# Kernel optimization log

Measured on AMD Instinct MI355X. Metric: run time of the kernel, lower is better.

The kernel has to match this reference:

```python
import jax, jax.numpy as jnp
import numpy as np

EPS = 1e-06

def _splat_dists(t, centers):
    # t: [B,T,H,Dh], centers: [H,S,Dh] -> euclidean dists [B,T,H,S] (torch.cdist)
    t_sq = jnp.sum(t * t, axis=-1, keepdims=True)          # [B,T,H,1]
    c_sq = jnp.sum(centers * centers, axis=-1)             # [H,S]
    dots = jnp.einsum('bthd,hsd->bths', t, centers)        # [B,T,H,S]
    d2 = jnp.maximum(t_sq + c_sq[None, None] - 2.0 * dots, 0.0)
    return jnp.sqrt(d2)


def setup_inputs() -> dict:
    key = jax.random.key(0)
    ks = jax.random.split(key, 6)
    B, T, D, H, S = 2, 2048, 1024, 8, 32
    Dh = D // H
    scale = 1.0 / np.sqrt(D)
    return {
        'x': jax.random.normal(ks[0], (B, T, D), jnp.float32),
        'Wqkv': jax.random.normal(ks[1], (D, 3 * D), jnp.float32) * scale,
        'bqkv': jnp.zeros((3 * D,), jnp.float32),
        'Wout': jax.random.normal(ks[2], (D, D), jnp.float32) * scale,
        'bout': jnp.zeros((D,), jnp.float32),
        'splat_centers': jax.random.normal(ks[3], (H, S, Dh), jnp.float32) * 0.5,
        'splat_log_scales': jnp.zeros((H, S), jnp.float32),
        'splat_log_amplitudes': jnp.zeros((H, S), jnp.float32),
        'temperature': jnp.ones((1,), jnp.float32),
    }


def reference(x, Wqkv, bqkv, Wout, bout, splat_centers, splat_log_scales,
              splat_log_amplitudes, temperature):
    B, T, D = x.shape
    H, S, Dh = splat_centers.shape
    qkv = (x @ Wqkv + bqkv).reshape(B, T, 3, H, Dh)
    q, k, v = qkv[:, :, 0], qkv[:, :, 1], qkv[:, :, 2]     # [B,T,H,Dh]

    q_dists = _splat_dists(q, splat_centers)               # [B,T,H,S]
    k_dists = _splat_dists(k, splat_centers)               # [B,T,H,S]

    scales = jnp.exp(splat_log_scales)[None, None]         # [1,1,H,S]
    q_weights = jnp.exp(-0.5 * (q_dists / (scales + EPS)) ** 2)
    k_weights = jnp.exp(-0.5 * (k_dists / (scales + EPS)) ** 2)

    amplitudes = jnp.exp(splat_log_amplitudes)             # [H,S]
    # bihs,bjhs,hs -> bijh : fold amplitudes into q_weights first
    qa = q_weights * amplitudes[None, None]
    logits = jnp.einsum('bihs,bjhs->bijh', qa, k_weights) / temperature[0]
    attention = jax.nn.softmax(logits, axis=2)             # softmax over j
    out = jnp.einsum('bijh,bjhd->bihd', attention, v).reshape(B, T, D)
    return out @ Wout + bout, attention
```

## Files before the change

kernel.cpp:

```cpp
#include <hip/hip_runtime.h>
#include <math.h>


typedef __attribute__((ext_vector_type(8))) short s16x8;
typedef __attribute__((ext_vector_type(4))) short s16x4;
typedef __attribute__((ext_vector_type(4))) float f32x4;

__device__ inline short f2bf(float f) {
  union { float f; unsigned u; } v; v.f = f;
  unsigned r = v.u + 0x7FFFu + ((v.u >> 16) & 1u);
  return (short)(r >> 16);
}
__device__ inline float bf2f(short s) {
  union { unsigned u; float f; } v;
  v.u = ((unsigned)(unsigned short)s) << 16;
  return v.f;
}
__device__ inline unsigned cvt_pk_bf16(float lo, float hi) {
  unsigned r;
  asm("v_cvt_pk_bf16_f32 %0, %1, %2" : "=v"(r) : "v"(lo), "v"(hi));
  return r;
}
#define MFMA_BF16(a, b, c) __builtin_amdgcn_mfma_f32_16x16x32_bf16((a), (b), (c), 0, 0, 0)

#define GLOAD_LDS16(gsrc, ldst)                                          \
  __builtin_amdgcn_global_load_lds(                                      \
      (const __attribute__((address_space(1))) void*)(gsrc),             \
      (__attribute__((address_space(3))) void*)(ldst), 16, 0, 0)

__device__ inline void transpose_tile32(const float* __restrict__ W,
                                        short* __restrict__ Wt, int K, int N,
                                        int n0, int k0) {
  __shared__ float tile[32][33];
  const int r = threadIdx.x >> 3, c4 = (threadIdx.x & 7) * 4;
  float4 v = *(const float4*)(W + (size_t)(k0 + r) * N + n0 + c4);
  tile[r][c4 + 0] = v.x; tile[r][c4 + 1] = v.y;
  tile[r][c4 + 2] = v.z; tile[r][c4 + 3] = v.w;
  __syncthreads();
  s16x4 o;
  o[0] = f2bf(tile[c4 + 0][r]);
  o[1] = f2bf(tile[c4 + 1][r]);
  o[2] = f2bf(tile[c4 + 2][r]);
  o[3] = f2bf(tile[c4 + 3][r]);
  *(s16x4*)(Wt + (size_t)(n0 + r) * K + k0 + c4) = o;
}

__global__ __launch_bounds__(256) void prep_fused(
    const float* __restrict__ x, short* __restrict__ x16,
    const float* __restrict__ Wqkv, short* __restrict__ Wqt16,
    const float* __restrict__ Wout, short* __restrict__ Wot16,
    const float* __restrict__ ctr, const float* __restrict__ ls,
    const float* __restrict__ la, short* __restrict__ c16,
    float* __restrict__ csq, float* __restrict__ inv2, float* __restrict__ amp) {
  const int bx = blockIdx.x;
  if (bx < 4096) {
    int i = bx * 256 + threadIdx.x;
    float4 v = ((const float4*)x)[i];
    s16x4 o;
    o[0] = f2bf(v.x); o[1] = f2bf(v.y); o[2] = f2bf(v.z); o[3] = f2bf(v.w);
    ((s16x4*)x16)[i] = o;
  } else if (bx < 7168) {
    int idx = bx - 4096;
    transpose_tile32(Wqkv, Wqt16, 1024, 3072, (idx % 96) * 32, (idx / 96) * 32);
  } else if (bx < 8192) {
    int idx = bx - 7168;
    transpose_tile32(Wout, Wot16, 1024, 1024, (idx % 32) * 32, (idx / 32) * 32);
  } else {
    const int t = threadIdx.x;
    float sumsq = 0.f;
#pragma unroll
    for (int d = 0; d < 128; d += 4) {
      float4 v = *(const float4*)(ctr + (size_t)t * 128 + d);
      sumsq += v.x * v.x + v.y * v.y + v.z * v.z + v.w * v.w;
      s16x4 o;
      o[0] = f2bf(v.x); o[1] = f2bf(v.y); o[2] = f2bf(v.z); o[3] = f2bf(v.w);
      *(s16x4*)(c16 + (size_t)t * 128 + d) = o;
    }
    csq[t] = sumsq;
    float sc = __expf(ls[t]);
    float iv = 1.0f / (sc + 1e-6f);
    inv2[t] = -0.5f * iv * iv;
    amp[t] = __expf(la[t]);
  }
}

template <int N, bool SCATTER>
__global__ __launch_bounds__(256) void gemm_bf16(
    const short* __restrict__ A, const short* __restrict__ Wt,
    const float* __restrict__ bias,
    short* __restrict__ q16, short* __restrict__ k16, short* __restrict__ vt16,
    float* __restrict__ outf) {
  __shared__ union {
    struct { short As[128 * 64]; short Bs[128 * 64]; } s;
    short tv[128 * 136];
  } sm;
  const int tid = threadIdx.x;
  const int w = tid >> 6, l = tid & 63;
  const int lm = l & 15, lk = l >> 4;
  const int bn0 = blockIdx.x * 128;
  const int bm0 = blockIdx.y * 128;
  const int n0 = bn0 + (w & 1) * 64;
  const int m0 = bm0 + (w >> 1) * 64;
  const int K = 1024;
  f32x4 acc[4][4];
#pragma unroll
  for (int mi = 0; mi < 4; mi++)
#pragma unroll
    for (int ni = 0; ni < 4; ni++) acc[mi][ni] = (f32x4){0.f, 0.f, 0.f, 0.f};

  const int srow = l >> 3;
  const int scol = (l & 7) * 8;
  const int mh = (w >> 1) * 64, nh = (w & 1) * 64;

  for (int k0 = 0; k0 < K; k0 += 64) {
#pragma unroll
    for (int q = 0; q < 4; q++) {
      const int chunk = w * 4 + q;
      const int row = chunk * 8 + srow;
      GLOAD_LDS16(A + (size_t)(bm0 + row) * K + k0 + scol, sm.s.As + chunk * 512);
      GLOAD_LDS16(Wt + (size_t)(bn0 + row) * K + k0 + scol, sm.s.Bs + chunk * 512);
    }
    __syncthreads();
#pragma unroll
    for (int kk = 0; kk < 2; kk++) {
      s16x8 af[4], bf[4];
#pragma unroll
      for (int i = 0; i < 4; i++) {
        af[i] = *(const s16x8*)(sm.s.As + (mh + i * 16 + lm) * 64 + kk * 32 + lk * 8);
        bf[i] = *(const s16x8*)(sm.s.Bs + (nh + i * 16 + lm) * 64 + kk * 32 + lk * 8);
      }
#pragma unroll
      for (int mi = 0; mi < 4; mi++)
#pragma unroll
        for (int ni = 0; ni < 4; ni++)
          acc[mi][ni] = MFMA_BF16(af[mi], bf[ni], acc[mi][ni]);
    }
    __syncthreads();
  }
  if (SCATTER) {
    const int three = bn0 >> 10;
    if (three < 2) {
      short* dst0 = three ? k16 : q16;
      const int h = (bn0 >> 7) & 7;
      const int bb = bm0 >> 11;
      const int bh = bb * 8 + h;
      const int tt0 = bm0 & 2047;
#pragma unroll
      for (int ni = 0; ni < 4; ni++) {
        const int n = n0 + ni * 16 + lm;
        const int dh = n & 127;
        const float bv = bias[n];
#pragma unroll
        for (int mi = 0; mi < 4; mi++) {
#pragma unroll
          for (int r = 0; r < 4; r++) {
            const int ml = mh + mi * 16 + lk * 4 + r;
            dst0[((size_t)bh * 2048 + tt0 + ml) * 128 + dh] =
                f2bf(acc[mi][ni][r] + bv);
          }
        }
      }
    } else {
      const int h = (bn0 >> 7) & 7;
      const int bb = bm0 >> 11;
      const int bh = bb * 8 + h;
      const int tt0 = bm0 & 2047;
#pragma unroll
      for (int ni = 0; ni < 4; ni++) {
        const int nl = nh + ni * 16 + lm;
        const float bv = bias[bn0 + nl];
#pragma unroll
        for (int mi = 0; mi < 4; mi++) {
          const int ml = mh + mi * 16 + lk * 4;
          s16x4 o;
          o[0] = f2bf(acc[mi][ni][0] + bv);
          o[1] = f2bf(acc[mi][ni][1] + bv);
          o[2] = f2bf(acc[mi][ni][2] + bv);
          o[3] = f2bf(acc[mi][ni][3] + bv);
          *(s16x4*)(sm.tv + nl * 136 + ml) = o;
        }
      }
      __syncthreads();
#pragma unroll
      for (int c = 0; c < 8; c++) {
        const int u = c * 256 + tid;
        const int n = u >> 4, ch = u & 15;
        s16x8 vv = *(const s16x8*)(sm.tv + n * 136 + ch * 8);
        *(s16x8*)(vt16 + ((size_t)(bh * 128 + n)) * 2048 + tt0 + ch * 8) = vv;
      }
    }
  } else {
#pragma unroll
    for (int ni = 0; ni < 4; ni++) {
      const int n = n0 + ni * 16 + lm;
      const float bv = bias[n];
#pragma unroll
      for (int mi = 0; mi < 4; mi++) {
#pragma unroll
        for (int r = 0; r < 4; r++) {
          const int m = m0 + mi * 16 + lk * 4 + r;
          outf[(size_t)m * N + n] = acc[mi][ni][r] + bv;
        }
      }
    }
  }
}

__global__ __launch_bounds__(256) void splat_tv(
    const short* __restrict__ q16, const short* __restrict__ k16,
    const short* __restrict__ c16, const float* __restrict__ csq,
    const float* __restrict__ inv2, const float* __restrict__ amp,
    short* __restrict__ qa16, short* __restrict__ kw16) {
  const int tid = threadIdx.x;
  const int it = blockIdx.x & 31;
  const int bh = (blockIdx.x >> 5) & 15;
  const int which = blockIdx.x >> 9;
  const int w = tid >> 6, l = tid & 63;
  const int lm = l & 15, lk = l >> 4;
  const int h = bh & 7;
  const int i0 = it * 64 + w * 16;
  const short* src = which ? k16 : q16;

  s16x8 af[4];
  float sq = 0.f;
#pragma unroll
  for (int kk = 0; kk < 4; kk++) {
    af[kk] = *(const s16x8*)(src + ((size_t)bh * 2048 + i0 + lm) * 128 + kk * 32 + lk * 8);
#pragma unroll
    for (int j = 0; j < 8; j++) {
      float f = bf2f(af[kk][j]);
      sq += f * f;
    }
  }
  sq += __shfl_xor(sq, 16);
  sq += __shfl_xor(sq, 32);

  f32x4 acc[2];
  acc[0] = (f32x4){0.f, 0.f, 0.f, 0.f};
  acc[1] = (f32x4){0.f, 0.f, 0.f, 0.f};
#pragma unroll
  for (int kk = 0; kk < 4; kk++) {
    s16x8 b0 = *(const s16x8*)(c16 + (size_t)(h * 32 + lm) * 128 + kk * 32 + lk * 8);
    s16x8 b1 = *(const s16x8*)(c16 + (size_t)(h * 32 + 16 + lm) * 128 + kk * 32 + lk * 8);
    acc[0] = MFMA_BF16(af[kk], b0, acc[0]);
    acc[1] = MFMA_BF16(af[kk], b1, acc[1]);
  }
  short* dst = which ? kw16 : qa16;
#pragma unroll
  for (int ni = 0; ni < 2; ni++) {
    const int n = ni * 16 + lm;
    const float cs = csq[h * 32 + n];
    const float iv2 = inv2[h * 32 + n];
    const float am = which ? 1.0f : amp[h * 32 + n];
#pragma unroll
    for (int r = 0; r < 4; r++) {
      float qs = __shfl(sq, lk * 4 + r);
      float d2 = fmaxf(qs + cs - 2.0f * acc[ni][r], 0.0f);
      float wv = __expf(iv2 * d2) * am;
      int m = i0 + lk * 4 + r;
      dst[((size_t)bh * 2048 + m) * 32 + n] = f2bf(wv);
    }
  }
}

__global__ __launch_bounds__(256) void attn_flash(
    const short* __restrict__ qa16, const short* __restrict__ kw16,
    const short* __restrict__ vt16, const float* __restrict__ temp,
    float* __restrict__ lrow, short* __restrict__ aout16) {
  __shared__ short Vs[2][8192];
  const int tid = threadIdx.x;
  const int w = tid >> 6, l = tid & 63;
  const int lm = l & 15, lk = l >> 4;
  const int it = blockIdx.x, h = blockIdx.y;
  const int b = blockIdx.z;
  const int bh = b * 8 + h;
  const int i0 = it * 64 + w * 16;
  const float invT = 1.0f / temp[0];
  const short* kwb = kw16 + (size_t)bh * 2048 * 32;
  const short* vtb = vt16 + (size_t)bh * 128 * 2048;
  s16x8 qfrag = *(const s16x8*)(qa16 + ((size_t)(bh * 2048 + i0 + lm)) * 32 + lk * 8);
  float lsum = 0.f;
  f32x4 acc[8];
#pragma unroll
  for (int d = 0; d < 8; d++) acc[d] = (f32x4){0.f, 0.f, 0.f, 0.f};

  const int sig0 = (lm >> 2) * 8 + (lm & 3);
  const int srow8 = l >> 3;
  const int scb = (l & 7) ^ srow8;
  const int rcb0 = (lk ^ (lm & 7)) * 8;
  const int rcb1 = ((lk + 4) ^ (lm & 7)) * 8;

#pragma unroll
  for (int q = 0; q < 4; q++) {
    const int chunk = w * 4 + q;
    GLOAD_LDS16(vtb + (size_t)(chunk * 8 + srow8) * 2048 + scb * 8,
                &Vs[0][chunk * 512]);
  }
  __syncthreads();

  int cur = 0;
  for (int jc = 0; jc < 2048; jc += 64) {
    if (jc + 64 < 2048) {
#pragma unroll
      for (int q = 0; q < 4; q++) {
        const int chunk = w * 4 + q;
        GLOAD_LDS16(vtb + (size_t)(chunk * 8 + srow8) * 2048 + (jc + 64) + scb * 8,
                    &Vs[cur ^ 1][chunk * 512]);
      }
    }
    s16x8 kb[4];
    kb[0] = *(const s16x8*)(kwb + (size_t)(jc + sig0) * 32 + lk * 8);
    kb[1] = *(const s16x8*)(kwb + (size_t)(jc + sig0 + 4) * 32 + lk * 8);
    kb[2] = *(const s16x8*)(kwb + (size_t)(jc + sig0 + 32) * 32 + lk * 8);
    kb[3] = *(const s16x8*)(kwb + (size_t)(jc + sig0 + 36) * 32 + lk * 8);
    f32x4 z = (f32x4){0.f, 0.f, 0.f, 0.f};
    f32x4 s[4];
#pragma unroll
    for (int c = 0; c < 4; c++) s[c] = MFMA_BF16(kb[c], qfrag, z);
    float p[4][4];
#pragma unroll
    for (int c = 0; c < 4; c++) {
      p[c][0] = __expf(s[c][0] * invT);
      p[c][1] = __expf(s[c][1] * invT);
      p[c][2] = __expf(s[c][2] * invT);
      p[c][3] = __expf(s[c][3] * invT);
      lsum += (p[c][0] + p[c][1]) + (p[c][2] + p[c][3]);
    }
    union { unsigned u[4]; s16x8 v; } t0, t1;
    t0.u[0] = cvt_pk_bf16(p[0][0], p[0][1]);
    t0.u[1] = cvt_pk_bf16(p[0][2], p[0][3]);
    t0.u[2] = cvt_pk_bf16(p[1][0], p[1][1]);
    t0.u[3] = cvt_pk_bf16(p[1][2], p[1][3]);
    t1.u[0] = cvt_pk_bf16(p[2][0], p[2][1]);
    t1.u[1] = cvt_pk_bf16(p[2][2], p[2][3]);
    t1.u[2] = cvt_pk_bf16(p[3][0], p[3][1]);
    t1.u[3] = cvt_pk_bf16(p[3][2], p[3][3]);
    s16x8 pf0 = t0.v, pf1 = t1.v;
    const short* vb = Vs[cur];
#pragma unroll
    for (int d = 0; d < 8; d++) {
      const short* vsrow = vb + (d * 16 + lm) * 64;
      s16x8 vb0 = *(const s16x8*)(vsrow + rcb0);
      s16x8 vb1 = *(const s16x8*)(vsrow + rcb1);
      acc[d] = MFMA_BF16(pf0, vb0, acc[d]);
      acc[d] = MFMA_BF16(pf1, vb1, acc[d]);
    }
    __syncthreads();
    cur ^= 1;
  }
  lsum += __shfl_xor(lsum, 16);
  lsum += __shfl_xor(lsum, 32);
  if (l < 16) lrow[bh * 2048 + i0 + l] = lsum;
  float invl[4];
#pragma unroll
  for (int r = 0; r < 4; r++) invl[r] = 1.0f / __shfl(lsum, lk * 4 + r);
  short* ob = aout16 + ((size_t)(b * 2048 + i0)) * 1024 + h * 128 + lm;
#pragma unroll
  for (int r = 0; r < 4; r++) {
    const int row = lk * 4 + r;
#pragma unroll
    for (int d = 0; d < 8; d++)
      ob[(size_t)row * 1024 + d * 16] = f2bf(acc[d][r] * invl[r]);
  }
}

__global__ __launch_bounds__(256) void gemm_out(
    const short* __restrict__ aout16, const short* __restrict__ Wot16,
    const float* __restrict__ bout, float* __restrict__ out) {
  __shared__ short As[128 * 64];
  __shared__ short Bs[64 * 64];
  const int tid = threadIdx.x;
  const int w = tid >> 6, l = tid & 63;
  const int lm = l & 15, lk = l >> 4;
  const int idx = blockIdx.x;
  const int bn0 = (idx & 15) * 64;
  const int bm0 = (idx >> 4) * 128;
  const int K = 1024;
  f32x4 acc[4][2];
#pragma unroll
  for (int mi = 0; mi < 4; mi++)
#pragma unroll
    for (int ni = 0; ni < 2; ni++) acc[mi][ni] = (f32x4){0.f, 0.f, 0.f, 0.f};
  const int srow = l >> 3;
  const int scol = (l & 7) * 8;
  const int mh = (w >> 1) * 64, nh = (w & 1) * 32;
  for (int k0 = 0; k0 < K; k0 += 64) {
#pragma unroll
    for (int q = 0; q < 4; q++) {
      const int chunk = w * 4 + q;
      GLOAD_LDS16(aout16 + (size_t)(bm0 + chunk * 8 + srow) * K + k0 + scol,
                  As + chunk * 512);
    }
#pragma unroll
    for (int q = 0; q < 2; q++) {
      const int chunk = w * 2 + q;
      GLOAD_LDS16(Wot16 + (size_t)(bn0 + chunk * 8 + srow) * K + k0 + scol,
                  Bs + chunk * 512);
    }
    __syncthreads();
#pragma unroll
    for (int kk = 0; kk < 2; kk++) {
      s16x8 af[4], bf[2];
#pragma unroll
      for (int i = 0; i < 4; i++)
        af[i] = *(const s16x8*)(As + (mh + i * 16 + lm) * 64 + kk * 32 + lk * 8);
#pragma unroll
      for (int i = 0; i < 2; i++)
        bf[i] = *(const s16x8*)(Bs + (nh + i * 16 + lm) * 64 + kk * 32 + lk * 8);
#pragma unroll
      for (int mi = 0; mi < 4; mi++)
#pragma unroll
        for (int ni = 0; ni < 2; ni++)
          acc[mi][ni] = MFMA_BF16(af[mi], bf[ni], acc[mi][ni]);
    }
    __syncthreads();
  }
#pragma unroll
  for (int ni = 0; ni < 2; ni++) {
    const int n = bn0 + nh + ni * 16 + lm;
    const float bv = bout[n];
#pragma unroll
    for (int mi = 0; mi < 4; mi++) {
#pragma unroll
      for (int r = 0; r < 4; r++) {
        const int m = bm0 + mh + mi * 16 + lk * 4 + r;
        out[(size_t)m * 1024 + n] = acc[mi][ni][r] + bv;
      }
    }
  }
}

__global__ __launch_bounds__(256) void attn_write(
    const short* __restrict__ qa16, const short* __restrict__ kw16,
    const float* __restrict__ lrow, const float* __restrict__ temp,
    float* __restrict__ attn) {
  __shared__ float pl[8][16][33];
  const int tid = threadIdx.x;
  const int w = tid >> 6, l = tid & 63;
  const int lm = l & 15, lk = l >> 4;
  const int bx = blockIdx.x;
  const int i0 = (bx & 127) * 16;
  const int j0 = ((bx >> 7) & 63) * 32;
  const int b = bx >> 13;
  const float invT = 1.0f / temp[0];
#pragma unroll
  for (int hh = 0; hh < 2; hh++) {
    const int h = w * 2 + hh;
    const int bh = b * 8 + h;
    s16x8 qf = *(const s16x8*)(qa16 + ((size_t)(bh * 2048 + i0 + lm)) * 32 + lk * 8);
    s16x8 kf[2];
#pragma unroll
    for (int jh = 0; jh < 2; jh++)
      kf[jh] = *(const s16x8*)(kw16 + ((size_t)(bh * 2048 + j0 + jh * 16 + lm)) * 32 + lk * 8);
    float il[4];
#pragma unroll
    for (int r = 0; r < 4; r++)
      il[r] = 1.0f / lrow[bh * 2048 + i0 + lk * 4 + r];
    f32x4 z = (f32x4){0.f, 0.f, 0.f, 0.f};
#pragma unroll
    for (int jh = 0; jh < 2; jh++) {
      f32x4 s = MFMA_BF16(qf, kf[jh], z);
#pragma unroll
      for (int r = 0; r < 4; r++) {
        float p = __expf(s[r] * invT) * il[r];
        pl[h][lk * 4 + r][jh * 16 + lm] = p;
      }
    }
  }
  __syncthreads();
#pragma unroll
  for (int c = 0; c < 4; c++) {
    int u = c * 256 + tid;
    int i = u >> 6, rem = u & 63;
    int j = rem >> 1, h4 = (rem & 1) * 4;
    f32x4 v;
    v[0] = pl[h4][i][j];
    v[1] = pl[h4 + 1][i][j];
    v[2] = pl[h4 + 2][i][j];
    v[3] = pl[h4 + 3][i][j];
    f32x4* dst = (f32x4*)(attn + (((size_t)(b * 2048 + i0 + i)) * 2048 + j0 + j) * 8 + h4);
    __builtin_nontemporal_store(v, dst);
  }
}

extern "C" void kernel_launch(void* const* d_in, const int* in_sizes, int n_in,
                              void* d_out, int out_size, void* d_ws, size_t ws_size,
                              hipStream_t stream) {
  const float* x    = (const float*)d_in[0];
  const float* Wqkv = (const float*)d_in[1];
  const float* bqkv = (const float*)d_in[2];
  const float* Wout = (const float*)d_in[3];
  const float* bout = (const float*)d_in[4];
  const float* ctr  = (const float*)d_in[5];
  const float* ls   = (const float*)d_in[6];
  const float* la   = (const float*)d_in[7];
  const float* temp = (const float*)d_in[8];

  float* out = (float*)d_out;
  float* attn = out + 4194304;

  short* ws16 = (short*)d_ws;
  short* q16   = ws16;
  short* k16   = q16 + 4194304;
  short* vt16  = k16 + 4194304;
  short* x16   = vt16 + 4194304;
  short* Wqt16 = x16 + 4194304;
  short* Wot16 = Wqt16 + 3145728;
  short* qa16  = Wot16 + 1048576;
  short* kw16  = qa16 + 1048576;
  short* aout16 = kw16 + 1048576;
  short* c16   = aout16 + 4194304;
  float* lrow  = (float*)(c16 + 32768);
  float* csq   = lrow + 32768;
  float* inv2  = csq + 256;
  float* amp   = inv2 + 256;

  prep_fused<<<8193, 256, 0, stream>>>(x, x16, Wqkv, Wqt16, Wout, Wot16,
                                       ctr, ls, la, c16, csq, inv2, amp);
  gemm_bf16<3072, true><<<dim3(24, 32), 256, 0, stream>>>(
      x16, Wqt16, bqkv, q16, k16, vt16, nullptr);
  splat_tv<<<1024, 256, 0, stream>>>(
      q16, k16, c16, csq, inv2, amp, qa16, kw16);
  attn_flash<<<dim3(32, 8, 2), 256, 0, stream>>>(
      qa16, kw16, vt16, temp, lrow, aout16);
  gemm_out<<<512, 256, 0, stream>>>(aout16, Wot16, bout, out);
  attn_write<<<16384, 256, 0, stream>>>(qa16, kw16, lrow, temp, attn);
}
```

Before: 453.8 us.

## Fuse splat distance/weight computation into QKV GEMM epilogue

```diff
diff --git a/kernel.cpp b/kernel.cpp
--- a/kernel.cpp
+++ b/kernel.cpp
@@ -84,12 +84,13 @@
   }
 }
 
-template <int N, bool SCATTER>
-__global__ __launch_bounds__(256) void gemm_bf16(
+__global__ __launch_bounds__(256) void gemm_qkv(
     const short* __restrict__ A, const short* __restrict__ Wt,
     const float* __restrict__ bias,
-    short* __restrict__ q16, short* __restrict__ k16, short* __restrict__ vt16,
-    float* __restrict__ outf) {
+    const short* __restrict__ c16, const float* __restrict__ csq,
+    const float* __restrict__ inv2, const float* __restrict__ amp,
+    short* __restrict__ qa16, short* __restrict__ kw16,
+    short* __restrict__ vt16) {
   __shared__ union {
     struct { short As[128 * 64]; short Bs[128 * 64]; } s;
     short tv[128 * 136];
@@ -99,8 +100,6 @@
   const int lm = l & 15, lk = l >> 4;
   const int bn0 = blockIdx.x * 128;
   const int bm0 = blockIdx.y * 128;
-  const int n0 = bn0 + (w & 1) * 64;
-  const int m0 = bm0 + (w >> 1) * 64;
   const int K = 1024;
   f32x4 acc[4][4];
 #pragma unroll
@@ -137,128 +136,94 @@
     }
     __syncthreads();
   }
-  if (SCATTER) {
-    const int three = bn0 >> 10;
-    if (three < 2) {
-      short* dst0 = three ? k16 : q16;
-      const int h = (bn0 >> 7) & 7;
-      const int bb = bm0 >> 11;
-      const int bh = bb * 8 + h;
-      const int tt0 = bm0 & 2047;
-#pragma unroll
-      for (int ni = 0; ni < 4; ni++) {
-        const int n = n0 + ni * 16 + lm;
-        const int dh = n & 127;
-        const float bv = bias[n];
-#pragma unroll
-        for (int mi = 0; mi < 4; mi++) {
-#pragma unroll
-          for (int r = 0; r < 4; r++) {
-            const int ml = mh + mi * 16 + lk * 4 + r;
-            dst0[((size_t)bh * 2048 + tt0 + ml) * 128 + dh] =
-                f2bf(acc[mi][ni][r] + bv);
-          }
+
+  const int three = bn0 >> 10;
+  const int h = (bn0 >> 7) & 7;
+  const int bb = bm0 >> 11;
+  const int bh = bb * 8 + h;
+  const int tt0 = bm0 & 2047;
+
+  if (three < 2) {
+#pragma unroll
+    for (int ni = 0; ni < 4; ni++) {
+      const int nl = nh + ni * 16 + lm;
+      const float bv = bias[bn0 + nl];
+#pragma unroll
+      for (int mi = 0; mi < 4; mi++) {
+#pragma unroll
+        for (int r = 0; r < 4; r++) {
+          const int ml = mh + mi * 16 + lk * 4 + r;
+          sm.tv[ml * 136 + nl] = f2bf(acc[mi][ni][r] + bv);
         }
       }
-    } else {
-      const int h = (bn0 >> 7) & 7;
-      const int bb = bm0 >> 11;
-      const int bh = bb * 8 + h;
-      const int tt0 = bm0 & 2047;
-#pragma unroll
-      for (int ni = 0; ni < 4; ni++) {
-        const int nl = nh + ni * 16 + lm;
-        const float bv = bias[bn0 + nl];
-#pragma unroll
-        for (int mi = 0; mi < 4; mi++) {
-          const int ml = mh + mi * 16 + lk * 4;
-          s16x4 o;
-          o[0] = f2bf(acc[mi][ni][0] + bv);
-          o[1] = f2bf(acc[mi][ni][1] + bv);
-          o[2] = f2bf(acc[mi][ni][2] + bv);
-          o[3] = f2bf(acc[mi][ni][3] + bv);
-          *(s16x4*)(sm.tv + nl * 136 + ml) = o;
+    }
+    __syncthreads();
+    short* dst = three ? kw16 : qa16;
+#pragma unroll
+    for (int sub = 0; sub < 2; sub++) {
+      const int iw = w * 32 + sub * 16;
+      s16x8 af[4];
+      float sq = 0.f;
+#pragma unroll
+      for (int kk = 0; kk < 4; kk++) {
+        af[kk] = *(const s16x8*)(sm.tv + (iw + lm) * 136 + kk * 32 + lk * 8);
+#pragma unroll
+        for (int j = 0; j < 8; j++) {
+          float f = bf2f(af[kk][j]);
+          sq += f * f;
         }
       }
-      __syncthreads();
-#pragma unroll
-      for (int c = 0; c < 8; c++) {
-        const int u = c * 256 + tid;
-        const int n = u >> 4, ch = u & 15;
-        s16x8 vv = *(const s16x8*)(sm.tv + n * 136 + ch * 8);
-        *(s16x8*)(vt16 + ((size_t)(bh * 128 + n)) * 2048 + tt0 + ch * 8) = vv;
+      sq += __shfl_xor(sq, 16);
+      sq += __shfl_xor(sq, 32);
+      f32x4 acc2[2];
+      acc2[0] = (f32x4){0.f, 0.f, 0.f, 0.f};
+      acc2[1] = (f32x4){0.f, 0.f, 0.f, 0.f};
+#pragma unroll
+      for (int kk = 0; kk < 4; kk++) {
+        s16x8 b0 = *(const s16x8*)(c16 + (size_t)(h * 32 + lm) * 128 + kk * 32 + lk * 8);
+        s16x8 b1 = *(const s16x8*)(c16 + (size_t)(h * 32 + 16 + lm) * 128 + kk * 32 + lk * 8);
+        acc2[0] = MFMA_BF16(af[kk], b0, acc2[0]);
+        acc2[1] = MFMA_BF16(af[kk], b1, acc2[1]);
+      }
+#pragma unroll
+      for (int ni = 0; ni < 2; ni++) {
+        const int n = ni * 16 + lm;
+        const float cs = csq[h * 32 + n];
+        const float iv2 = inv2[h * 32 + n];
+        const float am = three ? 1.0f : amp[h * 32 + n];
+#pragma unroll
+        for (int r = 0; r < 4; r++) {
+          float qs = __shfl(sq, lk * 4 + r);
+          float d2 = fmaxf(qs + cs - 2.0f * acc2[ni][r], 0.0f);
+          float wv = __expf(iv2 * d2) * am;
+          const int m = tt0 + iw + lk * 4 + r;
+          dst[((size_t)bh * 2048 + m) * 32 + n] = f2bf(wv);
+        }
       }
     }
   } else {
 #pragma unroll
     for (int ni = 0; ni < 4; ni++) {
-      const int n = n0 + ni * 16 + lm;
-      const float bv = bias[n];
+      const int nl = nh + ni * 16 + lm;
+      const float bv = bias[bn0 + nl];
 #pragma unroll
       for (int mi = 0; mi < 4; mi++) {
-#pragma unroll
-        for (int r = 0; r < 4; r++) {
-          const int m = m0 + mi * 16 + lk * 4 + r;
-          outf[(size_t)m * N + n] = acc[mi][ni][r] + bv;
-        }
-      }
-    }
-  }
-}
-
-__global__ __launch_bounds__(256) void splat_tv(
-    const short* __restrict__ q16, const short* __restrict__ k16,
-    const short* __restrict__ c16, const float* __restrict__ csq,
-    const float* __restrict__ inv2, const float* __restrict__ amp,
-    short* __restrict__ qa16, short* __restrict__ kw16) {
-  const int tid = threadIdx.x;
-  const int it = blockIdx.x & 31;
-  const int bh = (blockIdx.x >> 5) & 15;
-  const int which = blockIdx.x >> 9;
-  const int w = tid >> 6, l = tid & 63;
-  const int lm = l & 15, lk = l >> 4;
-  const int h = bh & 7;
-  const int i0 = it * 64 + w * 16;
-  const short* src = which ? k16 : q16;
-
-  s16x8 af[4];
-  float sq = 0.f;
-#pragma unroll
-  for (int kk = 0; kk < 4; kk++) {
-    af[kk] = *(const s16x8*)(src + ((size_t)bh * 2048 + i0 + lm) * 128 + kk * 32 + lk * 8);
-#pragma unroll
-    for (int j = 0; j < 8; j++) {
-      float f = bf2f(af[kk][j]);
-      sq += f * f;
-    }
-  }
-  sq += __shfl_xor(sq, 16);
-  sq += __shfl_xor(sq, 32);
-
-  f32x4 acc[2];
-  acc[0] = (f32x4){0.f, 0.f, 0.f, 0.f};
-  acc[1] = (f32x4){0.f, 0.f, 0.f, 0.f};
-#pragma unroll
-  for (int kk = 0; kk < 4; kk++) {
-    s16x8 b0 = *(const s16x8*)(c16 + (size_t)(h * 32 + lm) * 128 + kk * 32 + lk * 8);
-    s16x8 b1 = *(const s16x8*)(c16 + (size_t)(h * 32 + 16 + lm) * 128 + kk * 32 + lk * 8);
-    acc[0] = MFMA_BF16(af[kk], b0, acc[0]);
-    acc[1] = MFMA_BF16(af[kk], b1, acc[1]);
-  }
-  short* dst = which ? kw16 : qa16;
-#pragma unroll
-  for (int ni = 0; ni < 2; ni++) {
-    const int n = ni * 16 + lm;
-    const float cs = csq[h * 32 + n];
-    const float iv2 = inv2[h * 32 + n];
-    const float am = which ? 1.0f : amp[h * 32 + n];
-#pragma unroll
-    for (int r = 0; r < 4; r++) {
-      float qs = __shfl(sq, lk * 4 + r);
-      float d2 = fmaxf(qs + cs - 2.0f * acc[ni][r], 0.0f);
-      float wv = __expf(iv2 * d2) * am;
-      int m = i0 + lk * 4 + r;
-      dst[((size_t)bh * 2048 + m) * 32 + n] = f2bf(wv);
+        const int ml = mh + mi * 16 + lk * 4;
+        s16x4 o;
+        o[0] = f2bf(acc[mi][ni][0] + bv);
+        o[1] = f2bf(acc[mi][ni][1] + bv);
+        o[2] = f2bf(acc[mi][ni][2] + bv);
+        o[3] = f2bf(acc[mi][ni][3] + bv);
+        *(s16x4*)(sm.tv + nl * 136 + ml) = o;
+      }
+    }
+    __syncthreads();
+#pragma unroll
+    for (int c = 0; c < 8; c++) {
+      const int u = c * 256 + tid;
+      const int n = u >> 4, ch = u & 15;
+      s16x8 vv = *(const s16x8*)(sm.tv + n * 136 + ch * 8);
+      *(s16x8*)(vt16 + ((size_t)(bh * 128 + n)) * 2048 + tt0 + ch * 8) = vv;
     }
   }
 }
@@ -500,9 +465,7 @@
   float* attn = out + 4194304;
 
   short* ws16 = (short*)d_ws;
-  short* q16   = ws16;
-  short* k16   = q16 + 4194304;
-  short* vt16  = k16 + 4194304;
+  short* vt16  = ws16;
   short* x16   = vt16 + 4194304;
   short* Wqt16 = x16 + 4194304;
   short* Wot16 = Wqt16 + 3145728;
@@ -517,10 +480,8 @@
 
   prep_fused<<<8193, 256, 0, stream>>>(x, x16, Wqkv, Wqt16, Wout, Wot16,
                                        ctr, ls, la, c16, csq, inv2, amp);
-  gemm_bf16<3072, true><<<dim3(24, 32), 256, 0, stream>>>(
-      x16, Wqt16, bqkv, q16, k16, vt16, nullptr);
-  splat_tv<<<1024, 256, 0, stream>>>(
-      q16, k16, c16, csq, inv2, amp, qa16, kw16);
+  gemm_qkv<<<dim3(24, 32), 256, 0, stream>>>(
+      x16, Wqt16, bqkv, c16, csq, inv2, amp, qa16, kw16, vt16);
   attn_flash<<<dim3(32, 8, 2), 256, 0, stream>>>(
       qa16, kw16, vt16, temp, lrow, aout16);
   gemm_out<<<512, 256, 0, stream>>>(aout16, Wot16, bout, out);
```

After: 448.7 us. About the same (-1.1%).
